# Kernel tuning notes

Hardware: AMD Instinct MI355X
Metric: run time of the kernel (lower is better)

The kernel has to match this reference:

```python
import jax, jax.numpy as jnp
import numpy as np

N_NEURONS, D_MODEL, D_FF, N_PATTERNS, K_PATTERNS = 2048, 1024, 4096, 64, 4
B, S, K = 4, 2048, 8


def setup_inputs() -> dict:
    key = jax.random.key(0)
    ks = jax.random.split(key, 10)
    return {
        "x": jax.random.normal(ks[0], (B, S, D_MODEL), jnp.float32),
        "router_out": jax.random.normal(ks[1], (B, S, D_MODEL), jnp.float32),
        "topk_neuron_idx": jax.random.randint(ks[2], (B, S, K), 0, N_NEURONS),
        "topk_neuron_weights": jax.random.uniform(ks[3], (B, S, K), jnp.float32),
        "selected_neurons": jax.random.normal(ks[4], (B, S, K, D_MODEL), jnp.float32),
        "pattern_queries": jax.random.normal(ks[5], (N_PATTERNS, D_MODEL), jnp.float32) * 0.02,
        "gates": jax.random.normal(ks[6], (N_PATTERNS, D_FF), jnp.float32) * 0.02,
        "up_w": jax.random.normal(ks[7], (D_FF, D_MODEL), jnp.float32) / np.sqrt(D_MODEL),
        "up_b": jnp.zeros((D_FF,), jnp.float32),
        "down_w": jax.random.normal(ks[8], (D_MODEL, D_FF), jnp.float32) / np.sqrt(D_FF),
        "down_b": jnp.zeros((D_MODEL,), jnp.float32),
    }


def reference(x, router_out, topk_neuron_idx, topk_neuron_weights, selected_neurons,
              pattern_queries, gates, up_w, up_b, down_w, down_b):
    D = selected_neurons.shape[-1]
    # pattern scoring: [P, B, S, K]
    sim = jnp.einsum('pd,bskd->pbsk', pattern_queries, selected_neurons) / jnp.sqrt(jnp.float32(D))
    pattern_scores = jnp.einsum('pbsk,bsk->bsp', sim, topk_neuron_weights)  # weighted sum over K, permuted
    topk_scores, topk_pattern_idx = jax.lax.top_k(pattern_scores, K_PATTERNS)  # [B,S,k]
    topk_pattern_weights = jax.nn.softmax(topk_scores, axis=-1)
    selected_gates = gates[topk_pattern_idx]  # [B,S,k,d_ff]
    ffn_gate = jnp.einsum('bsk,bskf->bsf', topk_pattern_weights, selected_gates)
    h = jnp.einsum('bsd,fd->bsf', x, up_w) + up_b
    h = jax.nn.gelu(h * jax.nn.sigmoid(ffn_gate), approximate=False)
    return jnp.einsum('bsf,df->bsd', h, down_w) + down_b
```

## Files before the change

kernel.cpp:

```cpp
#include <hip/hip_runtime.h>
#include <hip/hip_bf16.h>
#include <math.h>

#define R_   8192
#define DM   1024
#define DFF  4096
#define NP   64
#define KN   8

typedef __bf16 bf16x8 __attribute__((ext_vector_type(8)));
typedef float  f32x4  __attribute__((ext_vector_type(4)));

__device__ __forceinline__ unsigned short f2bf(float f) {
  union { float f; unsigned u; } v; v.f = f;
  unsigned u = v.u;
  return (unsigned short)((u + 0x7FFFu + ((u >> 16) & 1u)) >> 16);
}

__device__ __forceinline__ float dot4(const float4 a, const float4 b) {
  return a.x * b.x + a.y * b.y + a.z * b.z + a.w * b.w;
}

__device__ __forceinline__ void fma4(float4& a, float w, const float4 s) {
  a.x += w * s.x; a.y += w * s.y; a.z += w * s.z; a.w += w * s.w;
}

__global__ __launch_bounds__(256) void cvt_bf16_kernel(
    const float* __restrict__ in, unsigned short* __restrict__ out, int n8) {
  int i = blockIdx.x * 256 + threadIdx.x;
  if (i >= n8) return;
  const float4* p = (const float4*)in + (size_t)i * 2;
  float4 a = p[0], b = p[1];
  uint4 r;
  r.x = (unsigned)f2bf(a.x) | ((unsigned)f2bf(a.y) << 16);
  r.y = (unsigned)f2bf(a.z) | ((unsigned)f2bf(a.w) << 16);
  r.z = (unsigned)f2bf(b.x) | ((unsigned)f2bf(b.y) << 16);
  r.w = (unsigned)f2bf(b.z) | ((unsigned)f2bf(b.w) << 16);
  ((uint4*)out)[i] = r;
}

__global__ __launch_bounds__(256, 2) void pattern_kernel(
    const float* __restrict__ sn,
    const float* __restrict__ tw,
    const float* __restrict__ pq,
    int*   __restrict__ out_idx,
    float* __restrict__ out_w)
{
  const int lane = threadIdx.x & 63;
  const int wave = threadIdx.x >> 6;
  const int pos0 = (blockIdx.x * 4 + wave) * 8;

  float4 vr[8][4];
#pragma unroll
  for (int p = 0; p < 8; ++p) {
    const int r = pos0 + p;
    const float* wp = tw + r * KN;
    const float* base = sn + (size_t)r * (KN * DM) + lane * 16;
    float4 a0 = {0,0,0,0}, a1 = {0,0,0,0}, a2 = {0,0,0,0}, a3 = {0,0,0,0};
#pragma unroll
    for (int k = 0; k < KN; ++k) {
      const float wk = wp[k];
      const float4* s = (const float4*)(base + k * DM);
      fma4(a0, wk, s[0]); fma4(a1, wk, s[1]);
      fma4(a2, wk, s[2]); fma4(a3, wk, s[3]);
    }
    vr[p][0] = a0; vr[p][1] = a1; vr[p][2] = a2; vr[p][3] = a3;
  }

  float sreg[8];
#pragma unroll 1
  for (int pat = 0; pat < NP; ++pat) {
    const float4* q = (const float4*)(pq + pat * DM + lane * 16);
    const float4 q0 = q[0], q1 = q[1], q2 = q[2], q3 = q[3];
    float part[8];
#pragma unroll
    for (int p = 0; p < 8; ++p)
      part[p] = dot4(q0, vr[p][0]) + dot4(q1, vr[p][1]) +
                dot4(q2, vr[p][2]) + dot4(q3, vr[p][3]);
#pragma unroll
    for (int off = 32; off >= 1; off >>= 1) {
#pragma unroll
      for (int p = 0; p < 8; ++p)
        part[p] += __shfl_xor(part[p], off, 64);
    }
    if (lane == pat) {
#pragma unroll
      for (int p = 0; p < 8; ++p) sreg[p] = part[p] * 0.03125f;
    }
  }

#pragma unroll
  for (int p = 0; p < 8; ++p) {
    float cur = sreg[p];
    float m0, m1, m2, m3; int i0, i1, i2, i3;
#define ARGMAX_STEP(MV, MI)                                   \
    {                                                         \
      float bv = cur; int bi = lane;                          \
      _Pragma("unroll")                                       \
      for (int off = 32; off >= 1; off >>= 1) {               \
        float ov = __shfl_xor(bv, off, 64);                   \
        int   oi = __shfl_xor(bi, off, 64);                   \
        if (ov > bv || (ov == bv && oi < bi)) { bv = ov; bi = oi; } \
      }                                                       \
      MV = bv; MI = bi;                                       \
      if (lane == bi) cur = -3.0e38f;                         \
    }
    ARGMAX_STEP(m0, i0) ARGMAX_STEP(m1, i1) ARGMAX_STEP(m2, i2) ARGMAX_STEP(m3, i3)
#undef ARGMAX_STEP
    const float e1 = __expf(m1 - m0), e2 = __expf(m2 - m0), e3 = __expf(m3 - m0);
    const float inv = 1.f / (1.f + e1 + e2 + e3);
    if (lane < 4) {
      const int r = pos0 + p;
      const int myi = (lane == 0) ? i0 : (lane == 1) ? i1 : (lane == 2) ? i2 : i3;
      const float mye = (lane == 0) ? 1.f : (lane == 1) ? e1 : (lane == 2) ? e2 : e3;
      out_idx[r * 4 + lane] = myi;
      out_w[r * 4 + lane] = mye * inv;
    }
  }
}

__device__ __forceinline__ void gll16(const void* g, void* l) {
  __builtin_amdgcn_global_load_lds(
      (const __attribute__((address_space(1))) unsigned int*)g,
      (__attribute__((address_space(3))) unsigned int*)l, 16, 0, 0);
}

template <int K, int N, int MODE>
__global__ __launch_bounds__(256, 2) void gemm_kernel(
    const unsigned short* __restrict__ A,
    const unsigned short* __restrict__ Bm,
    const float* __restrict__ bias,
    const int*   __restrict__ pidx,
    const float* __restrict__ pwt,
    const float* __restrict__ gates,
    void* __restrict__ Cout)
{
  __shared__ __align__(16) unsigned short As[128 * 32];
  __shared__ __align__(16) unsigned short Bs[128 * 32];
  const int tid  = threadIdx.x;
  const int lane = tid & 63;
  const int wid  = tid >> 6;
  const int wr   = wid >> 1;
  const int wc   = wid & 1;
  constexpr int NB = N / 128;
  const int brow = blockIdx.x / NB;
  const int bcol = blockIdx.x % NB;

  const unsigned short* Ab = A  + (size_t)brow * 128 * K;
  const unsigned short* Bb = Bm + (size_t)bcol * 128 * K;

  f32x4 acc[4][4];
#pragma unroll
  for (int m = 0; m < 4; ++m)
#pragma unroll
    for (int n = 0; n < 4; ++n)
      acc[m][n] = (f32x4){0.f, 0.f, 0.f, 0.f};

  const int srow = tid >> 2;
  const int scol = (tid & 3) * 8;
  char* ldsA = (char*)As + (tid >> 6) * 1024;
  char* ldsB = (char*)Bs + (tid >> 6) * 1024;

  const int arow = wr * 64 + (lane & 15);
  const int bro  = wc * 64 + (lane & 15);
  const int koff = (lane >> 4) * 8;

  for (int k0 = 0; k0 < K; k0 += 32) {
    if (k0) __syncthreads();
    gll16(Ab + (size_t)srow * K + k0 + scol,        ldsA);
    gll16(Ab + (size_t)(srow + 64) * K + k0 + scol, ldsA + 4096);
    gll16(Bb + (size_t)srow * K + k0 + scol,        ldsB);
    gll16(Bb + (size_t)(srow + 64) * K + k0 + scol, ldsB + 4096);
    __syncthreads();

    bf16x8 af[4], bfr[4];
#pragma unroll
    for (int m = 0; m < 4; ++m)
      af[m] = *(const bf16x8*)(As + (arow + m * 16) * 32 + koff);
#pragma unroll
    for (int n = 0; n < 4; ++n)
      bfr[n] = *(const bf16x8*)(Bs + (bro + n * 16) * 32 + koff);
#pragma unroll
    for (int m = 0; m < 4; ++m)
#pragma unroll
      for (int n = 0; n < 4; ++n)
        acc[m][n] = __builtin_amdgcn_mfma_f32_16x16x32_bf16(
            af[m], bfr[n], acc[m][n], 0, 0, 0);
  }

  const int crow0 = brow * 128 + wr * 64;
  const int ccol0 = bcol * 128 + wc * 64 + (lane & 15);
  const int rsub  = (lane >> 4) * 4;

  if (MODE == 0) {
    unsigned short* H = (unsigned short*)Cout;
#pragma unroll
    for (int m = 0; m < 4; ++m) {
      const int rbase = crow0 + m * 16 + rsub;
      int   ia[4][4];
      float wa[4][4];
#pragma unroll
      for (int j = 0; j < 4; ++j) {
        const int4   iq = *(const int4*)(pidx + (size_t)(rbase + j) * 4);
        const float4 wq = *(const float4*)(pwt + (size_t)(rbase + j) * 4);
        ia[j][0] = iq.x; ia[j][1] = iq.y; ia[j][2] = iq.z; ia[j][3] = iq.w;
        wa[j][0] = wq.x; wa[j][1] = wq.y; wa[j][2] = wq.z; wa[j][3] = wq.w;
      }
#pragma unroll
      for (int n = 0; n < 4; ++n) {
        const int col = ccol0 + n * 16;
        const float ub = bias[col];
#pragma unroll
        for (int j = 0; j < 4; ++j) {
          float g = wa[j][0] * gates[(size_t)ia[j][0] * DFF + col]
                  + wa[j][1] * gates[(size_t)ia[j][1] * DFF + col]
                  + wa[j][2] * gates[(size_t)ia[j][2] * DFF + col]
                  + wa[j][3] * gates[(size_t)ia[j][3] * DFF + col];
          const float u   = acc[m][n][j] + ub;
          const float val = u * (1.f / (1.f + __expf(-g)));
          const float h   = 0.5f * val * (1.f + erff(val * 0.70710678118654752f));
          H[(size_t)(rbase + j) * N + col] = f2bf(h);
        }
      }
    }
  } else {
    float* O = (float*)Cout;
#pragma unroll
    for (int m = 0; m < 4; ++m) {
      const int rbase = crow0 + m * 16 + rsub;
#pragma unroll
      for (int n = 0; n < 4; ++n) {
        const int col = ccol0 + n * 16;
        const float db = bias[col];
#pragma unroll
        for (int j = 0; j < 4; ++j)
          O[(size_t)(rbase + j) * N + col] = acc[m][n][j] + db;
      }
    }
  }
}

extern "C" void kernel_launch(void* const* d_in, const int* in_sizes, int n_in,
                              void* d_out, int out_size, void* d_ws, size_t ws_size,
                              hipStream_t stream) {
  const float* x     = (const float*)d_in[0];
  const float* tw    = (const float*)d_in[3];
  const float* sn    = (const float*)d_in[4];
  const float* pq    = (const float*)d_in[5];
  const float* gates = (const float*)d_in[6];
  const float* upw   = (const float*)d_in[7];
  const float* upb   = (const float*)d_in[8];
  const float* dnw   = (const float*)d_in[9];
  const float* dnb   = (const float*)d_in[10];
  float* out = (float*)d_out;

  char* p = (char*)d_ws;
  unsigned short* xb  = (unsigned short*)p; p += (size_t)R_ * DM * 2;
  unsigned short* uwb = (unsigned short*)p; p += (size_t)DFF * DM * 2;
  unsigned short* dwb = (unsigned short*)p; p += (size_t)DM * DFF * 2;
  unsigned short* H   = (unsigned short*)p; p += (size_t)R_ * DFF * 2;
  int*   pidx = (int*)p;   p += (size_t)R_ * 4 * sizeof(int);
  float* pwt  = (float*)p; p += (size_t)R_ * 4 * sizeof(float);

  cvt_bf16_kernel<<<(R_ * DM / 8) / 256, 256, 0, stream>>>(x, xb, R_ * DM / 8);
  cvt_bf16_kernel<<<(DFF * DM / 8) / 256, 256, 0, stream>>>(upw, uwb, DFF * DM / 8);
  cvt_bf16_kernel<<<(DM * DFF / 8) / 256, 256, 0, stream>>>(dnw, dwb, DM * DFF / 8);

  pattern_kernel<<<R_ / 32, 256, 0, stream>>>(sn, tw, pq, pidx, pwt);

  gemm_kernel<DM, DFF, 0><<<(R_ / 128) * (DFF / 128), 256, 0, stream>>>(
      xb, uwb, upb, pidx, pwt, gates, (void*)H);
  gemm_kernel<DFF, DM, 1><<<(R_ / 128) * (DM / 128), 256, 0, stream>>>(
      H, dwb, dnb, nullptr, nullptr, nullptr, (void*)out);
}
```

Baseline: 428.3 us.

## Split pattern scoring into weighted-sum and scoring kernels

The fused pattern kernel is split in two. The first kernel reduces the K selected neurons into a weighted vector per row, one block per row, and writes it to a workspace buffer. The second kernel reads those vectors and scores them against the 64 pattern queries with 4 rows per wave instead of 8, running twice as many blocks. The aim is more parallelism and better latency hiding on the 256 MB selected-neuron read, which was limited to 256 blocks. The cost is an extra 32 MB write and read of the intermediate buffer plus one more kernel launch.

```diff
diff --git a/kernel.cpp b/kernel.cpp
--- a/kernel.cpp
+++ b/kernel.cpp
@@ -39,58 +39,64 @@
   ((uint4*)out)[i] = r;
 }
 
-__global__ __launch_bounds__(256, 2) void pattern_kernel(
+__global__ __launch_bounds__(256) void vcomp_kernel(
     const float* __restrict__ sn,
     const float* __restrict__ tw,
+    float* __restrict__ v)
+{
+  const int r = blockIdx.x;
+  const int t = threadIdx.x;
+  float w[KN];
+#pragma unroll
+  for (int k = 0; k < KN; ++k) w[k] = tw[(size_t)r * KN + k];
+  const float* base = sn + (size_t)r * (KN * DM) + t * 4;
+  float4 a = {0.f, 0.f, 0.f, 0.f};
+#pragma unroll
+  for (int k = 0; k < KN; ++k) fma4(a, w[k], *(const float4*)(base + k * DM));
+  *(float4*)(v + (size_t)r * DM + t * 4) = a;
+}
+
+__global__ __launch_bounds__(256, 2) void score_kernel(
+    const float* __restrict__ v,
     const float* __restrict__ pq,
     int*   __restrict__ out_idx,
     float* __restrict__ out_w)
 {
   const int lane = threadIdx.x & 63;
   const int wave = threadIdx.x >> 6;
-  const int pos0 = (blockIdx.x * 4 + wave) * 8;
-
-  float4 vr[8][4];
-#pragma unroll
-  for (int p = 0; p < 8; ++p) {
-    const int r = pos0 + p;
-    const float* wp = tw + r * KN;
-    const float* base = sn + (size_t)r * (KN * DM) + lane * 16;
-    float4 a0 = {0,0,0,0}, a1 = {0,0,0,0}, a2 = {0,0,0,0}, a3 = {0,0,0,0};
-#pragma unroll
-    for (int k = 0; k < KN; ++k) {
-      const float wk = wp[k];
-      const float4* s = (const float4*)(base + k * DM);
-      fma4(a0, wk, s[0]); fma4(a1, wk, s[1]);
-      fma4(a2, wk, s[2]); fma4(a3, wk, s[3]);
-    }
-    vr[p][0] = a0; vr[p][1] = a1; vr[p][2] = a2; vr[p][3] = a3;
-  }
-
-  float sreg[8];
+  const int pos0 = (blockIdx.x * 4 + wave) * 4;
+
+  float4 vr[4][4];
+#pragma unroll
+  for (int p = 0; p < 4; ++p) {
+    const float4* s = (const float4*)(v + (size_t)(pos0 + p) * DM + lane * 16);
+    vr[p][0] = s[0]; vr[p][1] = s[1]; vr[p][2] = s[2]; vr[p][3] = s[3];
+  }
+
+  float sreg[4];
 #pragma unroll 1
   for (int pat = 0; pat < NP; ++pat) {
     const float4* q = (const float4*)(pq + pat * DM + lane * 16);
     const float4 q0 = q[0], q1 = q[1], q2 = q[2], q3 = q[3];
-    float part[8];
-#pragma unroll
-    for (int p = 0; p < 8; ++p)
+    float part[4];
+#pragma unroll
+    for (int p = 0; p < 4; ++p)
       part[p] = dot4(q0, vr[p][0]) + dot4(q1, vr[p][1]) +
                 dot4(q2, vr[p][2]) + dot4(q3, vr[p][3]);
 #pragma unroll
     for (int off = 32; off >= 1; off >>= 1) {
 #pragma unroll
-      for (int p = 0; p < 8; ++p)
+      for (int p = 0; p < 4; ++p)
         part[p] += __shfl_xor(part[p], off, 64);
     }
     if (lane == pat) {
 #pragma unroll
-      for (int p = 0; p < 8; ++p) sreg[p] = part[p] * 0.03125f;
-    }
-  }
-
-#pragma unroll
-  for (int p = 0; p < 8; ++p) {
+      for (int p = 0; p < 4; ++p) sreg[p] = part[p] * 0.03125f;
+    }
+  }
+
+#pragma unroll
+  for (int p = 0; p < 4; ++p) {
     float cur = sreg[p];
     float m0, m1, m2, m3; int i0, i1, i2, i3;
 #define ARGMAX_STEP(MV, MI)                                   \
@@ -261,12 +267,14 @@
   unsigned short* H   = (unsigned short*)p; p += (size_t)R_ * DFF * 2;
   int*   pidx = (int*)p;   p += (size_t)R_ * 4 * sizeof(int);
   float* pwt  = (float*)p; p += (size_t)R_ * 4 * sizeof(float);
+  float* vbuf = (float*)p; p += (size_t)R_ * DM * sizeof(float);
 
   cvt_bf16_kernel<<<(R_ * DM / 8) / 256, 256, 0, stream>>>(x, xb, R_ * DM / 8);
   cvt_bf16_kernel<<<(DFF * DM / 8) / 256, 256, 0, stream>>>(upw, uwb, DFF * DM / 8);
   cvt_bf16_kernel<<<(DM * DFF / 8) / 256, 256, 0, stream>>>(dnw, dwb, DM * DFF / 8);
 
-  pattern_kernel<<<R_ / 32, 256, 0, stream>>>(sn, tw, pq, pidx, pwt);
+  vcomp_kernel<<<R_, 256, 0, stream>>>(sn, tw, vbuf);
+  score_kernel<<<R_ / 16, 256, 0, stream>>>(vbuf, pq, pidx, pwt);
 
   gemm_kernel<DM, DFF, 0><<<(R_ / 128) * (DFF / 128), 256, 0, stream>>>(
       xb, uwb, upb, pidx, pwt, gates, (void*)H);
```

Result: faster. 408.5 us (-4.6%).
